# Kernel optimization log

Measured on AMD Instinct MI355X. Metric: run time of the kernel, lower is better.

The kernel has to match this reference:

```python
import jax, jax.numpy as jnp
import numpy as np

N, IN, OUT, H = 4096, 512, 64, 8
ALPHA = 0.2
NEG = -9e15


def glorot(key, shape):
    fan_in, fan_out = shape[-2], shape[-1]
    limit = np.sqrt(6.0 / (fan_in + fan_out))
    return jax.random.uniform(key, shape, jnp.float32, -limit, limit)


def setup_inputs() -> dict:
    key = jax.random.key(0)
    k1, k2, k3, k4, k5 = jax.random.split(key, 5)
    x = jax.random.normal(k1, (N, IN), jnp.float32)
    adj = jax.random.randint(k2, (N, N), 0, 2, jnp.int32)
    W = glorot(k3, (H, IN, OUT))            # stacked per-head kernels
    a1 = glorot(k4, (H, OUT, 1))[..., 0]    # [H, OUT] self attn vec
    a2 = glorot(k5, (H, OUT, 1))[..., 0]    # [H, OUT] neigh attn vec
    return {"x": x, "adj": adj, "W": W, "a1": a1, "a2": a2}


def reference(x, adj, W, a1, a2):
    # Wh: [H, N, OUT]
    Wh = jnp.einsum("ni,hio->hno", x, W)
    f1 = jnp.einsum("hno,ho->hn", Wh, a1)  # [H, N]
    f2 = jnp.einsum("hno,ho->hn", Wh, a2)  # [H, N]
    e = jax.nn.leaky_relu(f1[:, :, None] + f2[:, None, :], ALPHA)  # [H, N, N]
    e = jnp.where(adj[None] > 0, e, NEG)
    attn = jax.nn.softmax(e, axis=-1)       # dropout inactive (eval mode)
    h = jnp.einsum("hnm,hmo->hno", attn, Wh)  # [H, N, OUT]
    # concat heads along features -> [N, H*OUT]
    out = jnp.transpose(h, (1, 0, 2)).reshape(N, H * OUT)
    return out
```

## Files before the change

kernel.cpp:

```cpp
#include <hip/hip_runtime.h>
#include <hip/hip_bf16.h>
#include <stdint.h>


constexpr int N_ = 4096, IN_ = 512, OUT_ = 64, H_ = 8;
constexpr float ALPHA_ = 0.2f;

typedef __attribute__((ext_vector_type(8))) short short8;
typedef __attribute__((ext_vector_type(4))) float f32x4;

__device__ __forceinline__ uint32_t rne_pack2(float a, float b, float& ra, float& rb) {
    uint32_t ua = __float_as_uint(a); ua += 0x7fffu + ((ua >> 16) & 1u); ua >>= 16;
    uint32_t ub = __float_as_uint(b); ub += 0x7fffu + ((ub >> 16) & 1u); ub >>= 16;
    ra = __uint_as_float(ua << 16);
    rb = __uint_as_float(ub << 16);
    return ua | (ub << 16);
}

__global__ __launch_bounds__(256) void pack_adj(const int* __restrict__ adj,
                                                unsigned long long* __restrict__ bitsT) {
    size_t base = (size_t)blockIdx.x * 256 + threadIdx.x;
    const size_t stride = (size_t)4096 * 256;
#pragma unroll
    for (int it = 0; it < 16; it++) {
        size_t g = base + (size_t)it * stride;
        int v = adj[g];
        unsigned long long m = __ballot(v != 0);
        if ((threadIdx.x & 63) == 0) {
            int n = (int)(g >> 12);
            int c = (int)((g >> 6) & 63);
            bitsT[(size_t)c * N_ + n] = m;
        }
    }
}

__global__ __launch_bounds__(256) void split_x(const float* __restrict__ x,
                                               uint16_t* __restrict__ xh,
                                               uint16_t* __restrict__ xl) {
    size_t g = ((size_t)blockIdx.x * 256 + threadIdx.x) * 8;
    float4 v0 = *(const float4*)(x + g);
    float4 v1 = *(const float4*)(x + g + 4);
    float v[8] = {v0.x, v0.y, v0.z, v0.w, v1.x, v1.y, v1.z, v1.w};
    uint32_t ph[4], pl[4];
#pragma unroll
    for (int i = 0; i < 4; i++) {
        float h0, h1, d0, d1;
        ph[i] = rne_pack2(v[2 * i], v[2 * i + 1], h0, h1);
        pl[i] = rne_pack2(v[2 * i] - h0, v[2 * i + 1] - h1, d0, d1);
    }
    *(uint4*)(xh + g) = make_uint4(ph[0], ph[1], ph[2], ph[3]);
    *(uint4*)(xl + g) = make_uint4(pl[0], pl[1], pl[2], pl[3]);
}

__global__ __launch_bounds__(256) void split_wT(const float* __restrict__ W,
                                                uint16_t* __restrict__ WTh,
                                                uint16_t* __restrict__ WTl) {
    __shared__ float T[64 * 68];
    const int t  = threadIdx.x;
    const int kb = blockIdx.x;
    const int h  = blockIdx.y;
    {
        int kk = t >> 2, os = (t & 3) * 16;
        const float* src = W + ((size_t)h * IN_ + kb * 64 + kk) * OUT_ + os;
#pragma unroll
        for (int j = 0; j < 4; j++)
            *(float4*)&T[kk * 68 + os + j * 4] = *(const float4*)(src + j * 4);
    }
    __syncthreads();
    int o = t >> 2, ks = (t & 3) * 16;
    uint32_t ph[8], pl[8];
#pragma unroll
    for (int i = 0; i < 8; i++) {
        float va = T[(ks + 2 * i) * 68 + o], vb = T[(ks + 2 * i + 1) * 68 + o];
        float h0, h1, d0, d1;
        ph[i] = rne_pack2(va, vb, h0, h1);
        pl[i] = rne_pack2(va - h0, vb - h1, d0, d1);
    }
    size_t dst = ((size_t)h * OUT_ + o) * IN_ + kb * 64 + ks;
    *(uint4*)&WTh[dst]     = make_uint4(ph[0], ph[1], ph[2], ph[3]);
    *(uint4*)&WTh[dst + 8] = make_uint4(ph[4], ph[5], ph[6], ph[7]);
    *(uint4*)&WTl[dst]     = make_uint4(pl[0], pl[1], pl[2], pl[3]);
    *(uint4*)&WTl[dst + 8] = make_uint4(pl[4], pl[5], pl[6], pl[7]);
}

__global__ __launch_bounds__(256) void wh_mfma(const uint16_t* __restrict__ xh,
                                               const uint16_t* __restrict__ xl,
                                               const uint16_t* __restrict__ WTh,
                                               const uint16_t* __restrict__ WTl,
                                               const float* __restrict__ a1,
                                               const float* __restrict__ a2,
                                               uint16_t* __restrict__ WhhT,
                                               float* __restrict__ f1,
                                               float* __restrict__ f2) {
    __shared__ __align__(16) char ldsbuf[4 * 64 * 72 * 2];
    uint16_t* Ah = (uint16_t*)ldsbuf;
    uint16_t* Al = Ah + 64 * 72;
    uint16_t* Bh = Al + 64 * 72;
    uint16_t* Bl = Bh + 64 * 72;
    const int t  = threadIdx.x;
    const int h  = blockIdx.y;
    const int n0 = blockIdx.x * 64;
    const int l  = t & 63, w = t >> 6;
    const int p  = l & 15, q = l >> 4;
    const int sr = t >> 2, sc = (t & 3) * 16;

    f32x4 acc[4];
#pragma unroll
    for (int rt = 0; rt < 4; rt++) acc[rt] = (f32x4){0.f, 0.f, 0.f, 0.f};

    const uint16_t* gxh = xh + (size_t)(n0 + sr) * IN_ + sc;
    const uint16_t* gxl = xl + (size_t)(n0 + sr) * IN_ + sc;
    const uint16_t* gbh = WTh + ((size_t)h * OUT_ + sr) * IN_ + sc;
    const uint16_t* gbl = WTl + ((size_t)h * OUT_ + sr) * IN_ + sc;

    for (int kt = 0; kt < 8; kt++) {
        __syncthreads();
        uint4 a0 = *(const uint4*)(gxh + kt * 64);
        uint4 a1v = *(const uint4*)(gxh + kt * 64 + 8);
        uint4 b0 = *(const uint4*)(gxl + kt * 64);
        uint4 b1 = *(const uint4*)(gxl + kt * 64 + 8);
        uint4 c0 = *(const uint4*)(gbh + kt * 64);
        uint4 c1 = *(const uint4*)(gbh + kt * 64 + 8);
        uint4 d0 = *(const uint4*)(gbl + kt * 64);
        uint4 d1 = *(const uint4*)(gbl + kt * 64 + 8);
        *(uint4*)&Ah[sr * 72 + sc]     = a0;
        *(uint4*)&Ah[sr * 72 + sc + 8] = a1v;
        *(uint4*)&Al[sr * 72 + sc]     = b0;
        *(uint4*)&Al[sr * 72 + sc + 8] = b1;
        *(uint4*)&Bh[sr * 72 + sc]     = c0;
        *(uint4*)&Bh[sr * 72 + sc + 8] = c1;
        *(uint4*)&Bl[sr * 72 + sc]     = d0;
        *(uint4*)&Bl[sr * 72 + sc + 8] = d1;
        __syncthreads();
#pragma unroll
        for (int k0 = 0; k0 < 2; k0++) {
            short8 bhf = *(const short8*)&Bh[(w * 16 + p) * 72 + q * 8 + k0 * 32];
            short8 blf = *(const short8*)&Bl[(w * 16 + p) * 72 + q * 8 + k0 * 32];
#pragma unroll
            for (int rt = 0; rt < 4; rt++) {
                short8 ahf = *(const short8*)&Ah[(rt * 16 + p) * 72 + q * 8 + k0 * 32];
                short8 alf = *(const short8*)&Al[(rt * 16 + p) * 72 + q * 8 + k0 * 32];
                acc[rt] = __builtin_amdgcn_mfma_f32_16x16x32_bf16(ahf, bhf, acc[rt], 0, 0, 0);
                acc[rt] = __builtin_amdgcn_mfma_f32_16x16x32_bf16(alf, bhf, acc[rt], 0, 0, 0);
                acc[rt] = __builtin_amdgcn_mfma_f32_16x16x32_bf16(ahf, blf, acc[rt], 0, 0, 0);
            }
        }
    }
    __syncthreads();
    float* Whs = (float*)ldsbuf;
#pragma unroll
    for (int rt = 0; rt < 4; rt++)
#pragma unroll
        for (int reg = 0; reg < 4; reg++)
            Whs[(rt * 16 + q * 4 + reg) * 68 + w * 16 + p] = acc[rt][reg];
    __syncthreads();
    {
        int r = t >> 2, og = (t & 3) * 16;
        float s1 = 0.f, s2 = 0.f;
#pragma unroll
        for (int j = 0; j < 4; j++) {
            float4 wv = *(const float4*)&Whs[r * 68 + og + j * 4];
            float4 av = *(const float4*)(a1 + h * OUT_ + og + j * 4);
            float4 bv = *(const float4*)(a2 + h * OUT_ + og + j * 4);
            s1 += wv.x * av.x + wv.y * av.y + wv.z * av.z + wv.w * av.w;
            s2 += wv.x * bv.x + wv.y * bv.y + wv.z * bv.z + wv.w * bv.w;
        }
        s1 += __shfl_xor(s1, 1, 64); s1 += __shfl_xor(s1, 2, 64);
        s2 += __shfl_xor(s2, 1, 64); s2 += __shfl_xor(s2, 2, 64);
        if ((t & 3) == 0) {
            f1[(size_t)h * N_ + n0 + r] = s1;
            f2[(size_t)h * N_ + n0 + r] = s2;
        }
    }
    {
        int o = t >> 2, ns = (t & 3) * 16;
        uint32_t ph[8];
#pragma unroll
        for (int i = 0; i < 8; i++) {
            float va = Whs[(ns + 2 * i) * 68 + o], vb = Whs[(ns + 2 * i + 1) * 68 + o];
            float h0, h1;
            ph[i] = rne_pack2(va, vb, h0, h1);
        }
        size_t dst = ((size_t)h * OUT_ + o) * N_ + n0 + ns;
        *(uint4*)&WhhT[dst]     = make_uint4(ph[0], ph[1], ph[2], ph[3]);
        *(uint4*)&WhhT[dst + 8] = make_uint4(ph[4], ph[5], ph[6], ph[7]);
    }
}

__global__ __launch_bounds__(512, 4) void gat_main(const unsigned long long* __restrict__ bitsT,
                                                   const uint16_t* __restrict__ WhhT,
                                                   const float* __restrict__ f1,
                                                   const float* __restrict__ f2,
                                                   float* __restrict__ out) {
    __shared__ __align__(16) uint16_t Bh[2][2][64 * 72];
    const int t   = threadIdx.x;
    const int h   = blockIdx.y;
    const int n0  = blockIdx.x * 64;
    const int grp = t >> 8;
    const int tg  = t & 255;
    const int l   = t & 63;
    const int wg  = tg >> 6;
    const int p   = l & 15, q = l >> 4;
    const int sr  = tg >> 2, sc = (tg & 3) * 16;
    const int row = wg * 16 + p;

    const float f1v = f1[(size_t)h * N_ + n0 + row];
    const float* f2b = f2 + (size_t)h * N_ + (size_t)grp * 2048;
    const uint16_t* gb = WhhT + ((size_t)h * OUT_ + sr) * N_ + (size_t)grp * 2048 + sc;
    const unsigned long long* bp = bitsT + (size_t)(grp * 32) * N_ + n0 + row;

    float Lp = 0.f;
    f32x4 acc[4];
#pragma unroll
    for (int ct = 0; ct < 4; ct++) acc[ct] = (f32x4){0.f, 0.f, 0.f, 0.f};

    {
        uint4 b0 = *(const uint4*)(gb);
        uint4 b1 = *(const uint4*)(gb + 8);
        *(uint4*)&Bh[grp][0][sr * 72 + sc]     = b0;
        *(uint4*)&Bh[grp][0][sr * 72 + sc + 8] = b1;
    }
    unsigned long long word = bp[0];
    bp += N_;

    for (int cc = 0; cc < 32; cc++) {
        uint16_t* Bcur = Bh[grp][cc & 1];
        uint16_t* Bnxt = Bh[grp][(cc & 1) ^ 1];
        __syncthreads();
        uint4 nb0 = *(const uint4*)(gb + (cc + 1) * 64);
        uint4 nb1 = *(const uint4*)(gb + (cc + 1) * 64 + 8);
        unsigned long long nword = *bp;
        bp += N_;
        const float* fpc = f2b + cc * 64 + q * 8;
        float4 fa0 = *(const float4*)(fpc);
        float4 fa1 = *(const float4*)(fpc + 4);
        float4 fb0 = *(const float4*)(fpc + 32);
        float4 fb1 = *(const float4*)(fpc + 36);
#pragma unroll
        for (int k0 = 0; k0 < 2; k0++) {
            float fs[8];
            if (k0 == 0) {
                fs[0] = fa0.x; fs[1] = fa0.y; fs[2] = fa0.z; fs[3] = fa0.w;
                fs[4] = fa1.x; fs[5] = fa1.y; fs[6] = fa1.z; fs[7] = fa1.w;
            } else {
                fs[0] = fb0.x; fs[1] = fb0.y; fs[2] = fb0.z; fs[3] = fb0.w;
                fs[4] = fb1.x; fs[5] = fb1.y; fs[6] = fb1.z; fs[7] = fb1.w;
            }
            uint32_t bits8 = (uint32_t)(word >> (k0 * 32 + q * 8)) & 0xffu;
            float pv[8];
#pragma unroll
            for (int j = 0; j < 8; j++) {
                float s = f1v + fs[j];
                float e = fmaxf(s, ALPHA_ * s);
                float ex = __expf(e);
                uint32_t msk = (uint32_t)((int32_t)(bits8 << (31 - j)) >> 31);
                pv[j] = __uint_as_float(__float_as_uint(ex) & msk);
            }
            union { short8 s8; uint32_t u[4]; } af;
#pragma unroll
            for (int i = 0; i < 4; i++) {
                uint32_t pk;
                asm("v_cvt_pk_bf16_f32 %0, %1, %2"
                    : "=v"(pk)
                    : "v"(pv[2 * i]), "v"(pv[2 * i + 1]));
                af.u[i] = pk;
                Lp += __uint_as_float(pk << 16) + __uint_as_float(pk & 0xffff0000u);
            }
#pragma unroll
            for (int ct = 0; ct < 4; ct++) {
                short8 bhf = *(const short8*)&Bcur[(ct * 16 + p) * 72 + q * 8 + k0 * 32];
                acc[ct] = __builtin_amdgcn_mfma_f32_16x16x32_bf16(af.s8, bhf, acc[ct], 0, 0, 0);
            }
        }
        *(uint4*)&Bnxt[sr * 72 + sc]     = nb0;
        *(uint4*)&Bnxt[sr * 72 + sc + 8] = nb1;
        word = nword;
    }
    float Ls = Lp;
    Ls += __shfl_xor(Ls, 16, 64);
    Ls += __shfl_xor(Ls, 32, 64);

    __syncthreads();
    float* Red  = (float*)&Bh[0][0][0];
    float* Lsum = Red + 128;
    if (q == 0) Red[grp * 64 + row] = Ls;
    if (grp == 1) {
#pragma unroll
        for (int ct = 0; ct < 4; ct++)
#pragma unroll
            for (int reg = 0; reg < 4; reg++)
                Lsum[(wg * 16 + q * 4 + reg) * 68 + ct * 16 + p] = acc[ct][reg];
    }
    __syncthreads();
    if (grp == 0) {
        float inv[4];
#pragma unroll
        for (int reg = 0; reg < 4; reg++) {
            int rr = wg * 16 + q * 4 + reg;
            float L = Red[rr] + Red[64 + rr];
            inv[reg] = 1.f / L;
        }
#pragma unroll
        for (int ct = 0; ct < 4; ct++)
#pragma unroll
            for (int reg = 0; reg < 4; reg++) {
                int rr = wg * 16 + q * 4 + reg;
                float v = (acc[ct][reg] + Lsum[rr * 68 + ct * 16 + p]) * inv[reg];
                out[(size_t)(n0 + rr) * (H_ * OUT_) + h * OUT_ + ct * 16 + p] = v;
            }
    }
}

extern "C" void kernel_launch(void* const* d_in, const int* in_sizes, int n_in,
                              void* d_out, int out_size, void* d_ws, size_t ws_size,
                              hipStream_t stream) {
    const float* x   = nullptr;
    const int*   adj = nullptr;
    const float* W   = nullptr;
    const float* a1  = nullptr;
    const float* a2  = nullptr;
    for (int i = 0; i < n_in; i++) {
        long long sz = in_sizes[i];
        if      (sz == (long long)N_ * IN_)        x   = (const float*)d_in[i];
        else if (sz == (long long)N_ * N_)         adj = (const int*)d_in[i];
        else if (sz == (long long)H_ * IN_ * OUT_) W   = (const float*)d_in[i];
        else if (sz == (long long)H_ * OUT_) {
            if (!a1) a1 = (const float*)d_in[i];
            else     a2 = (const float*)d_in[i];
        }
    }
    if (!x)   x   = (const float*)d_in[0];
    if (!adj) adj = (const int*)d_in[1];
    if (!W)   W   = (const float*)d_in[2];
    if (!a1)  a1  = (const float*)d_in[3];
    if (!a2)  a2  = (const float*)d_in[4];
    float* out = (float*)d_out;

    char* ws = (char*)d_ws;
    unsigned long long* bitsT = (unsigned long long*)ws;
    uint16_t* WhhT = (uint16_t*)(ws + (2u  << 20));
    float* f1      = (float*)   (ws + (6u  << 20));
    float* f2      = (float*)   (ws + (6u  << 20) + (128u << 10));
    uint16_t* xh   = (uint16_t*)(ws + (6u  << 20) + (512u << 10));
    uint16_t* xl   = (uint16_t*)(ws + (10u << 20) + (512u << 10));
    uint16_t* WTh  = (uint16_t*)(ws + (14u << 20) + (512u << 10));
    uint16_t* WTl  = (uint16_t*)(ws + (15u << 20));

    pack_adj<<<4096, 256, 0, stream>>>(adj, bitsT);
    split_x<<<(N_ * IN_) / (256 * 8), 256, 0, stream>>>(x, xh, xl);
    split_wT<<<dim3(IN_ / 64, H_), 256, 0, stream>>>(W, WTh, WTl);
    wh_mfma<<<dim3(N_ / 64, H_), 256, 0, stream>>>(xh, xl, WTh, WTl, a1, a2, WhhT, f1, f2);
    gat_main<<<dim3(N_ / 64, H_), 512, 0, stream>>>(bitsT, WhhT, f1, f2, out);
}
```

Measured before the change: 201.4 us.

## Merge preprocessing kernels, deepen LDS ring, prefetch f2/mask, use packed FP32 math

The three preprocessing kernels (adjacency bit-packing, x split, W transpose/split) are merged into one launch dispatched by block index, removing two launch gaps. In gat_main the B tile buffer becomes a 4-slot ring with prefetch distance 2, which halves the number of block barriers. The f2 values and adjacency words are now prefetched one iteration ahead, and the LDS row pitch changes from 72 to 76. The leaky-relu arithmetic uses v_pk_add/v_pk_mul and sbfe for the mask bits. LDS use doubles, which may lower occupancy, and the prefetch reads past the end of each group's segment on the last iterations.

```diff
diff --git a/kernel.cpp b/kernel.cpp
--- a/kernel.cpp
+++ b/kernel.cpp
@@ -8,6 +8,7 @@
 
 typedef __attribute__((ext_vector_type(8))) short short8;
 typedef __attribute__((ext_vector_type(4))) float f32x4;
+typedef __attribute__((ext_vector_type(2))) float f32x2;
 
 __device__ __forceinline__ uint32_t rne_pack2(float a, float b, float& ra, float& rb) {
     uint32_t ua = __float_as_uint(a); ua += 0x7fffu + ((ua >> 16) & 1u); ua >>= 16;
@@ -17,70 +18,79 @@
     return ua | (ub << 16);
 }
 
-__global__ __launch_bounds__(256) void pack_adj(const int* __restrict__ adj,
-                                                unsigned long long* __restrict__ bitsT) {
-    size_t base = (size_t)blockIdx.x * 256 + threadIdx.x;
-    const size_t stride = (size_t)4096 * 256;
-#pragma unroll
-    for (int it = 0; it < 16; it++) {
-        size_t g = base + (size_t)it * stride;
-        int v = adj[g];
-        unsigned long long m = __ballot(v != 0);
-        if ((threadIdx.x & 63) == 0) {
-            int n = (int)(g >> 12);
-            int c = (int)((g >> 6) & 63);
-            bitsT[(size_t)c * N_ + n] = m;
-        }
-    }
-}
-
-__global__ __launch_bounds__(256) void split_x(const float* __restrict__ x,
-                                               uint16_t* __restrict__ xh,
-                                               uint16_t* __restrict__ xl) {
-    size_t g = ((size_t)blockIdx.x * 256 + threadIdx.x) * 8;
-    float4 v0 = *(const float4*)(x + g);
-    float4 v1 = *(const float4*)(x + g + 4);
-    float v[8] = {v0.x, v0.y, v0.z, v0.w, v1.x, v1.y, v1.z, v1.w};
-    uint32_t ph[4], pl[4];
-#pragma unroll
-    for (int i = 0; i < 4; i++) {
-        float h0, h1, d0, d1;
-        ph[i] = rne_pack2(v[2 * i], v[2 * i + 1], h0, h1);
-        pl[i] = rne_pack2(v[2 * i] - h0, v[2 * i + 1] - h1, d0, d1);
-    }
-    *(uint4*)(xh + g) = make_uint4(ph[0], ph[1], ph[2], ph[3]);
-    *(uint4*)(xl + g) = make_uint4(pl[0], pl[1], pl[2], pl[3]);
-}
-
-__global__ __launch_bounds__(256) void split_wT(const float* __restrict__ W,
-                                                uint16_t* __restrict__ WTh,
-                                                uint16_t* __restrict__ WTl) {
+__device__ __forceinline__ f32x2 pk_add(f32x2 a, f32x2 b) {
+    f32x2 d; asm("v_pk_add_f32 %0, %1, %2" : "=v"(d) : "v"(a), "v"(b)); return d;
+}
+__device__ __forceinline__ f32x2 pk_mul(f32x2 a, f32x2 b) {
+    f32x2 d; asm("v_pk_mul_f32 %0, %1, %2" : "=v"(d) : "v"(a), "v"(b)); return d;
+}
+
+__global__ __launch_bounds__(256) void preprocess(const int* __restrict__ adj,
+                                                  unsigned long long* __restrict__ bitsT,
+                                                  const float* __restrict__ x,
+                                                  uint16_t* __restrict__ xh,
+                                                  uint16_t* __restrict__ xl,
+                                                  const float* __restrict__ W,
+                                                  uint16_t* __restrict__ WTh,
+                                                  uint16_t* __restrict__ WTl) {
     __shared__ float T[64 * 68];
-    const int t  = threadIdx.x;
-    const int kb = blockIdx.x;
-    const int h  = blockIdx.y;
-    {
-        int kk = t >> 2, os = (t & 3) * 16;
-        const float* src = W + ((size_t)h * IN_ + kb * 64 + kk) * OUT_ + os;
-#pragma unroll
-        for (int j = 0; j < 4; j++)
-            *(float4*)&T[kk * 68 + os + j * 4] = *(const float4*)(src + j * 4);
-    }
-    __syncthreads();
-    int o = t >> 2, ks = (t & 3) * 16;
-    uint32_t ph[8], pl[8];
-#pragma unroll
-    for (int i = 0; i < 8; i++) {
-        float va = T[(ks + 2 * i) * 68 + o], vb = T[(ks + 2 * i + 1) * 68 + o];
-        float h0, h1, d0, d1;
-        ph[i] = rne_pack2(va, vb, h0, h1);
-        pl[i] = rne_pack2(va - h0, vb - h1, d0, d1);
-    }
-    size_t dst = ((size_t)h * OUT_ + o) * IN_ + kb * 64 + ks;
-    *(uint4*)&WTh[dst]     = make_uint4(ph[0], ph[1], ph[2], ph[3]);
-    *(uint4*)&WTh[dst + 8] = make_uint4(ph[4], ph[5], ph[6], ph[7]);
-    *(uint4*)&WTl[dst]     = make_uint4(pl[0], pl[1], pl[2], pl[3]);
-    *(uint4*)&WTl[dst + 8] = make_uint4(pl[4], pl[5], pl[6], pl[7]);
+    const int b = blockIdx.x;
+    if (b < 4096) {
+        size_t base = (size_t)b * 256 + threadIdx.x;
+        const size_t stride = (size_t)4096 * 256;
+#pragma unroll
+        for (int it = 0; it < 16; it++) {
+            size_t g = base + (size_t)it * stride;
+            int v = adj[g];
+            unsigned long long m = __ballot(v != 0);
+            if ((threadIdx.x & 63) == 0) {
+                int n = (int)(g >> 12);
+                int c = (int)((g >> 6) & 63);
+                bitsT[(size_t)c * N_ + n] = m;
+            }
+        }
+    } else if (b < 4096 + 1024) {
+        size_t g = ((size_t)(b - 4096) * 256 + threadIdx.x) * 8;
+        float4 v0 = *(const float4*)(x + g);
+        float4 v1 = *(const float4*)(x + g + 4);
+        float v[8] = {v0.x, v0.y, v0.z, v0.w, v1.x, v1.y, v1.z, v1.w};
+        uint32_t ph[4], pl[4];
+#pragma unroll
+        for (int i = 0; i < 4; i++) {
+            float h0, h1, d0, d1;
+            ph[i] = rne_pack2(v[2 * i], v[2 * i + 1], h0, h1);
+            pl[i] = rne_pack2(v[2 * i] - h0, v[2 * i + 1] - h1, d0, d1);
+        }
+        *(uint4*)(xh + g) = make_uint4(ph[0], ph[1], ph[2], ph[3]);
+        *(uint4*)(xl + g) = make_uint4(pl[0], pl[1], pl[2], pl[3]);
+    } else {
+        const int idx = b - 5120;
+        const int kb = idx & 7;
+        const int h  = idx >> 3;
+        const int t  = threadIdx.x;
+        {
+            int kk = t >> 2, os = (t & 3) * 16;
+            const float* src = W + ((size_t)h * IN_ + kb * 64 + kk) * OUT_ + os;
+#pragma unroll
+            for (int j = 0; j < 4; j++)
+                *(float4*)&T[kk * 68 + os + j * 4] = *(const float4*)(src + j * 4);
+        }
+        __syncthreads();
+        int o = t >> 2, ks = (t & 3) * 16;
+        uint32_t ph[8], pl[8];
+#pragma unroll
+        for (int i = 0; i < 8; i++) {
+            float va = T[(ks + 2 * i) * 68 + o], vb = T[(ks + 2 * i + 1) * 68 + o];
+            float h0, h1, d0, d1;
+            ph[i] = rne_pack2(va, vb, h0, h1);
+            pl[i] = rne_pack2(va - h0, vb - h1, d0, d1);
+        }
+        size_t dst = ((size_t)h * OUT_ + o) * IN_ + kb * 64 + ks;
+        *(uint4*)&WTh[dst]     = make_uint4(ph[0], ph[1], ph[2], ph[3]);
+        *(uint4*)&WTh[dst + 8] = make_uint4(ph[4], ph[5], ph[6], ph[7]);
+        *(uint4*)&WTl[dst]     = make_uint4(pl[0], pl[1], pl[2], pl[3]);
+        *(uint4*)&WTl[dst + 8] = make_uint4(pl[4], pl[5], pl[6], pl[7]);
+    }
 }
 
 __global__ __launch_bounds__(256) void wh_mfma(const uint16_t* __restrict__ xh,
@@ -192,7 +202,8 @@
                                                    const float* __restrict__ f1,
                                                    const float* __restrict__ f2,
                                                    float* __restrict__ out) {
-    __shared__ __align__(16) uint16_t Bh[2][2][64 * 72];
+    constexpr int LDB = 76;
+    __shared__ __align__(16) uint16_t Bh[2][4][64 * LDB];
     const int t   = threadIdx.x;
     const int h   = blockIdx.y;
     const int n0  = blockIdx.x * 64;
@@ -205,6 +216,8 @@
     const int row = wg * 16 + p;
 
     const float f1v = f1[(size_t)h * N_ + n0 + row];
+    const f32x2 f1v2 = {f1v, f1v};
+    const f32x2 al2  = {ALPHA_, ALPHA_};
     const float* f2b = f2 + (size_t)h * N_ + (size_t)grp * 2048;
     const uint16_t* gb = WhhT + ((size_t)h * OUT_ + sr) * N_ + (size_t)grp * 2048 + sc;
     const unsigned long long* bp = bitsT + (size_t)(grp * 32) * N_ + n0 + row;
@@ -215,66 +228,78 @@
     for (int ct = 0; ct < 4; ct++) acc[ct] = (f32x4){0.f, 0.f, 0.f, 0.f};
 
     {
-        uint4 b0 = *(const uint4*)(gb);
-        uint4 b1 = *(const uint4*)(gb + 8);
-        *(uint4*)&Bh[grp][0][sr * 72 + sc]     = b0;
-        *(uint4*)&Bh[grp][0][sr * 72 + sc + 8] = b1;
-    }
-    unsigned long long word = bp[0];
-    bp += N_;
+        uint4 a0 = *(const uint4*)(gb);
+        uint4 a1 = *(const uint4*)(gb + 8);
+        uint4 b0 = *(const uint4*)(gb + 64);
+        uint4 b1 = *(const uint4*)(gb + 64 + 8);
+        *(uint4*)&Bh[grp][0][sr * LDB + sc]     = a0;
+        *(uint4*)&Bh[grp][0][sr * LDB + sc + 8] = a1;
+        *(uint4*)&Bh[grp][1][sr * LDB + sc]     = b0;
+        *(uint4*)&Bh[grp][1][sr * LDB + sc + 8] = b1;
+    }
+    unsigned long long w_cur = bp[0];
+    float4 fca0, fca1, fcb0, fcb1;
+    {
+        const float* fpc = f2b + q * 8;
+        fca0 = *(const float4*)(fpc);
+        fca1 = *(const float4*)(fpc + 4);
+        fcb0 = *(const float4*)(fpc + 32);
+        fcb1 = *(const float4*)(fpc + 36);
+    }
+    __syncthreads();
 
     for (int cc = 0; cc < 32; cc++) {
-        uint16_t* Bcur = Bh[grp][cc & 1];
-        uint16_t* Bnxt = Bh[grp][(cc & 1) ^ 1];
-        __syncthreads();
-        uint4 nb0 = *(const uint4*)(gb + (cc + 1) * 64);
-        uint4 nb1 = *(const uint4*)(gb + (cc + 1) * 64 + 8);
-        unsigned long long nword = *bp;
-        bp += N_;
-        const float* fpc = f2b + cc * 64 + q * 8;
-        float4 fa0 = *(const float4*)(fpc);
-        float4 fa1 = *(const float4*)(fpc + 4);
-        float4 fb0 = *(const float4*)(fpc + 32);
-        float4 fb1 = *(const float4*)(fpc + 36);
+        if (cc && !(cc & 1)) __syncthreads();
+        uint4 nb0 = *(const uint4*)(gb + (cc + 2) * 64);
+        uint4 nb1 = *(const uint4*)(gb + (cc + 2) * 64 + 8);
+        unsigned long long w_nxt = bp[(size_t)(cc + 1) * N_];
+        const float* fpn = f2b + (cc + 1) * 64 + q * 8;
+        float4 fna0 = *(const float4*)(fpn);
+        float4 fna1 = *(const float4*)(fpn + 4);
+        float4 fnb0 = *(const float4*)(fpn + 32);
+        float4 fnb1 = *(const float4*)(fpn + 36);
+
+        const uint16_t* Bcur = &Bh[grp][cc & 3][0];
 #pragma unroll
         for (int k0 = 0; k0 < 2; k0++) {
-            float fs[8];
+            f32x2 fs2[4];
             if (k0 == 0) {
-                fs[0] = fa0.x; fs[1] = fa0.y; fs[2] = fa0.z; fs[3] = fa0.w;
-                fs[4] = fa1.x; fs[5] = fa1.y; fs[6] = fa1.z; fs[7] = fa1.w;
+                fs2[0] = (f32x2){fca0.x, fca0.y}; fs2[1] = (f32x2){fca0.z, fca0.w};
+                fs2[2] = (f32x2){fca1.x, fca1.y}; fs2[3] = (f32x2){fca1.z, fca1.w};
             } else {
-                fs[0] = fb0.x; fs[1] = fb0.y; fs[2] = fb0.z; fs[3] = fb0.w;
-                fs[4] = fb1.x; fs[5] = fb1.y; fs[6] = fb1.z; fs[7] = fb1.w;
-            }
-            uint32_t bits8 = (uint32_t)(word >> (k0 * 32 + q * 8)) & 0xffu;
-            float pv[8];
-#pragma unroll
-            for (int j = 0; j < 8; j++) {
-                float s = f1v + fs[j];
-                float e = fmaxf(s, ALPHA_ * s);
-                float ex = __expf(e);
-                uint32_t msk = (uint32_t)((int32_t)(bits8 << (31 - j)) >> 31);
-                pv[j] = __uint_as_float(__float_as_uint(ex) & msk);
-            }
+                fs2[0] = (f32x2){fcb0.x, fcb0.y}; fs2[1] = (f32x2){fcb0.z, fcb0.w};
+                fs2[2] = (f32x2){fcb1.x, fcb1.y}; fs2[3] = (f32x2){fcb1.z, fcb1.w};
+            }
+            uint32_t bits8 = (uint32_t)(w_cur >> (k0 * 32 + q * 8)) & 0xffu;
             union { short8 s8; uint32_t u[4]; } af;
 #pragma unroll
             for (int i = 0; i < 4; i++) {
+                f32x2 s2 = pk_add(f1v2, fs2[i]);
+                f32x2 t2 = pk_mul(al2, s2);
+                float e0 = fmaxf(s2.x, t2.x);
+                float e1 = fmaxf(s2.y, t2.y);
+                float ex0 = __expf(e0);
+                float ex1 = __expf(e1);
+                uint32_t m0 = (uint32_t)__builtin_amdgcn_sbfe((int)bits8, 2 * i, 1);
+                uint32_t m1 = (uint32_t)__builtin_amdgcn_sbfe((int)bits8, 2 * i + 1, 1);
+                float pv0 = __uint_as_float(__float_as_uint(ex0) & m0);
+                float pv1 = __uint_as_float(__float_as_uint(ex1) & m1);
                 uint32_t pk;
-                asm("v_cvt_pk_bf16_f32 %0, %1, %2"
-                    : "=v"(pk)
-                    : "v"(pv[2 * i]), "v"(pv[2 * i + 1]));
+                asm("v_cvt_pk_bf16_f32 %0, %1, %2" : "=v"(pk) : "v"(pv0), "v"(pv1));
                 af.u[i] = pk;
                 Lp += __uint_as_float(pk << 16) + __uint_as_float(pk & 0xffff0000u);
             }
 #pragma unroll
             for (int ct = 0; ct < 4; ct++) {
-                short8 bhf = *(const short8*)&Bcur[(ct * 16 + p) * 72 + q * 8 + k0 * 32];
+                short8 bhf = *(const short8*)&Bcur[(ct * 16 + p) * LDB + q * 8 + k0 * 32];
                 acc[ct] = __builtin_amdgcn_mfma_f32_16x16x32_bf16(af.s8, bhf, acc[ct], 0, 0, 0);
             }
         }
-        *(uint4*)&Bnxt[sr * 72 + sc]     = nb0;
-        *(uint4*)&Bnxt[sr * 72 + sc + 8] = nb1;
-        word = nword;
+        uint16_t* Bw = &Bh[grp][(cc + 2) & 3][0];
+        *(uint4*)&Bw[sr * LDB + sc]     = nb0;
+        *(uint4*)&Bw[sr * LDB + sc + 8] = nb1;
+        w_cur = w_nxt;
+        fca0 = fna0; fca1 = fna1; fcb0 = fnb0; fcb1 = fnb1;
     }
     float Ls = Lp;
     Ls += __shfl_xor(Ls, 16, 64);
@@ -346,9 +371,7 @@
     uint16_t* WTh  = (uint16_t*)(ws + (14u << 20) + (512u << 10));
     uint16_t* WTl  = (uint16_t*)(ws + (15u << 20));
 
-    pack_adj<<<4096, 256, 0, stream>>>(adj, bitsT);
-    split_x<<<(N_ * IN_) / (256 * 8), 256, 0, stream>>>(x, xh, xl);
-    split_wT<<<dim3(IN_ / 64, H_), 256, 0, stream>>>(W, WTh, WTl);
+    preprocess<<<4096 + 1024 + 64, 256, 0, stream>>>(adj, bitsT, x, xh, xl, W, WTh, WTl);
     wh_mfma<<<dim3(N_ / 64, H_), 256, 0, stream>>>(xh, xl, WTh, WTl, a1, a2, WhhT, f1, f2);
     gat_main<<<dim3(N_ / 64, H_), 512, 0, stream>>>(bitsT, WhhT, f1, f2, out);
 }
```

Measured after the change: 277.6 us. 1.38x slower.
